# Performance work log

Hardware: AMD Instinct MI355X
Metric: run time of the kernel (lower is better)

Reference implementation:

```python
import jax, jax.numpy as jnp
import numpy as np
import math

EMBED_DIM = 1024
NHEAD = 16
HD = EMBED_DIM // NHEAD      # 64
HHD = HD // 2                # 32
LAMBDA_INIT = 0.8
LN_EPS = 1e-5
B, T = 2, 2048


def setup_inputs() -> dict:
    key = jax.random.key(0)
    ks = jax.random.split(key, 12)
    d = EMBED_DIM
    inp = {
        "x": jax.random.normal(ks[0], (B, T, d), dtype=jnp.float32),
        "key_padding_mask": jnp.zeros((B, T), dtype=bool),
        "Wq": jax.random.normal(ks[1], (d, d), dtype=jnp.float32) / math.sqrt(d),
        "Wk": jax.random.normal(ks[2], (d, d), dtype=jnp.float32) / math.sqrt(d),
        "Wv": jax.random.normal(ks[3], (d, d), dtype=jnp.float32) / math.sqrt(d),
        "Wo": jax.random.normal(ks[4], (d, d), dtype=jnp.float32) / math.sqrt(d),
        "gamma": jnp.ones((d,), dtype=jnp.float32),
        "beta": jnp.zeros((d,), dtype=jnp.float32),
        "lq1": jax.random.normal(ks[5], (NHEAD, HHD), dtype=jnp.float32) * 0.1,
        "lk1": jax.random.normal(ks[6], (NHEAD, HHD), dtype=jnp.float32) * 0.1,
        "lq2": jax.random.normal(ks[7], (NHEAD, HHD), dtype=jnp.float32) * 0.1,
        "lk2": jax.random.normal(ks[8], (NHEAD, HHD), dtype=jnp.float32) * 0.1,
    }
    return inp


def _diff_attn(x, key_padding_mask, Wq, Wk, Wv, Wo, gamma, beta, lq1, lk1, lq2, lk2):
    b, t, d = x.shape
    scale = math.sqrt(HHD)

    def split(w):  # [B,T,D] -> [B,H,T,hd]
        return w.reshape(b, t, NHEAD, HD).transpose(0, 2, 1, 3)

    Q = split(x @ Wq.T)
    K = split(x @ Wk.T)
    V = split(x @ Wv.T)
    Q1, Q2 = Q[..., :HHD], Q[..., HHD:]
    K1, K2 = K[..., :HHD], K[..., HHD:]

    def attn(q, k):  # [B,H,T,hhd] x [B,H,T,hhd] -> softmax scores [B,H,T,T]
        scores = jnp.einsum('bhqe,bhke->bhqk', q, k) / scale
        scores = jnp.where(key_padding_mask[:, None, None, :], -jnp.inf, scores)
        return jax.nn.softmax(scores, axis=-1)

    lam = (jnp.exp(jnp.sum(lq1 * lk1, axis=-1))
           - jnp.exp(jnp.sum(lq2 * lk2, axis=-1))
           + LAMBDA_INIT)  # [H]
    A = attn(Q1, K1) - lam[None, :, None, None] * attn(Q2, K2)
    out = jnp.einsum('bhqk,bhkd->bhqd', A, V).transpose(0, 2, 1, 3).reshape(b, t, d)
    y = out @ Wo.T + x
    mu = jnp.mean(y, axis=-1, keepdims=True)
    var = jnp.mean((y - mu) ** 2, axis=-1, keepdims=True)
    return (y - mu) / jnp.sqrt(var + LN_EPS) * gamma + beta


def reference(x, key_padding_mask, Wq, Wk, Wv, Wo, gamma, beta, lq1, lk1, lq2, lk2):
    return _diff_attn(x, key_padding_mask, Wq, Wk, Wv, Wo, gamma, beta, lq1, lk1, lq2, lk2)
```

## Files before the change

### kernel.cpp

```cpp
#include <hip/hip_runtime.h>
#include <stdint.h>

#define DEVI __device__ __forceinline__

typedef __bf16 bf16x8 __attribute__((ext_vector_type(8)));
typedef float f32x4 __attribute__((ext_vector_type(4)));
typedef unsigned short u16x8 __attribute__((ext_vector_type(8)));
typedef unsigned u32x2 __attribute__((ext_vector_type(2)));
typedef unsigned u32x4 __attribute__((ext_vector_type(4)));

#define MFMA16(a, b, c) __builtin_amdgcn_mfma_f32_16x16x32_bf16((a), (b), (c), 0, 0, 0)

constexpr int EMBED = 1024;
constexpr int NHEADC = 16;
constexpr int BB = 2;
constexpr int TT = 2048;
constexpr int MROWS = BB * TT;
constexpr int QKSTR = 2048;
constexpr float QSCALE = 0.17677669529663687f * 1.4426950408889634f;

DEVI unsigned short f2bf(float f) {
  unsigned u = __float_as_uint(f);
  u += 0x7fffu + ((u >> 16) & 1u);
  return (unsigned short)(u >> 16);
}
DEVI unsigned cvtpk(float lo, float hi) {
  unsigned pk;
  asm("v_cvt_pk_bf16_f32 %0, %1, %2" : "=v"(pk) : "v"(lo), "v"(hi));
  return pk;
}

DEVI void gl2lds16(const void* g, void* l) {
  __builtin_amdgcn_global_load_lds(
      (const __attribute__((address_space(1))) void*)(uintptr_t)g,
      (__attribute__((address_space(3))) void*)(unsigned)(uintptr_t)l,
      16, 0, 0);
}

DEVI void split_body(const float* in, unsigned short* hi, int n4, int start, int stride) {
  for (int i = start; i < n4; i += stride) {
    float4 v = reinterpret_cast<const float4*>(in)[i];
    ushort4 h;
    h.x = f2bf(v.x); h.y = f2bf(v.y); h.z = f2bf(v.z); h.w = f2bf(v.w);
    reinterpret_cast<ushort4*>(hi)[i] = h;
  }
}

__global__ __launch_bounds__(256) void k_split(const float* __restrict__ in,
                                               unsigned short* __restrict__ hi, int n4) {
  split_body(in, hi, n4, blockIdx.x * blockDim.x + threadIdx.x, gridDim.x * blockDim.x);
}

__global__ __launch_bounds__(256) void k_splitw(
    const float* __restrict__ Wq, const float* __restrict__ Wk,
    const float* __restrict__ Wv, const float* __restrict__ Wo,
    unsigned short* __restrict__ wqkv, unsigned short* __restrict__ woh) {
  const int y = blockIdx.y;
  const int n4 = EMBED * EMBED / 4;
  const float* in = (y == 0) ? Wq : (y == 1) ? Wk : (y == 2) ? Wv : Wo;
  unsigned short* hi =
      (y == 3) ? woh : wqkv + (size_t)y * EMBED * EMBED;
  split_body(in, hi, n4, blockIdx.x * blockDim.x + threadIdx.x, gridDim.x * blockDim.x);
}

template <int EPI>
__global__ __launch_bounds__(256) void k_gemm(
    const unsigned short* __restrict__ Ahi, const unsigned short* __restrict__ Bhi,
    unsigned short* __restrict__ O1, unsigned short* __restrict__ O2,
    float* __restrict__ Of32, const float* __restrict__ resid,
    int M, int N, int K, int ldo, float oscale) {
  __shared__ __align__(16) unsigned short sAh[128 * 64];
  __shared__ __align__(16) unsigned short sBh[128 * 64];

  const int tid = threadIdx.x;
  const int lane = tid & 63;
  const int w = tid >> 6;
  const int arow = lane & 15;
  const int g = lane >> 4;
  const int bm = blockIdx.y * 128;
  const int bn = blockIdx.x * 128;
  const int wr = (w >> 1) * 64;
  const int wc = (w & 1) * 64;

  const f32x4 z4 = {0.f, 0.f, 0.f, 0.f};
  f32x4 acc[4][4];
#pragma unroll
  for (int i = 0; i < 4; ++i)
#pragma unroll
    for (int j = 0; j < 4; ++j) acc[i][j] = z4;

  for (int k0 = 0; k0 < K; k0 += 64) {
    __syncthreads();
#pragma unroll
    for (int i = 0; i < 4; ++i) {
      const int cid = (i * 4 + w) * 64 + lane;
      const int r = cid >> 3;
      const int c = cid & 7;
      const int sc = (c ^ (r & 7)) * 8;
      const int ldso = (i * 4 + w) * 512;
      gl2lds16(Ahi + (size_t)(bm + r) * K + k0 + sc, &sAh[ldso]);
      gl2lds16(Bhi + (size_t)(bn + r) * K + k0 + sc, &sBh[ldso]);
    }
    __syncthreads();
#pragma unroll
    for (int kk = 0; kk < 2; ++kk) {
      bf16x8 ah[4], bh[4];
#pragma unroll
      for (int mi = 0; mi < 4; ++mi) {
        const int row = wr + mi * 16 + arow;
        const int ch = ((kk * 4 + g) ^ (row & 7)) * 8;
        ah[mi] = *reinterpret_cast<const bf16x8*>(&sAh[row * 64 + ch]);
      }
#pragma unroll
      for (int ni = 0; ni < 4; ++ni) {
        const int row = wc + ni * 16 + arow;
        const int ch = ((kk * 4 + g) ^ (row & 7)) * 8;
        bh[ni] = *reinterpret_cast<const bf16x8*>(&sBh[row * 64 + ch]);
      }
#pragma unroll
      for (int mi = 0; mi < 4; ++mi)
#pragma unroll
        for (int ni = 0; ni < 4; ++ni)
          acc[mi][ni] = MFMA16(ah[mi], bh[ni], acc[mi][ni]);
    }
  }

#pragma unroll
  for (int mi = 0; mi < 4; ++mi)
#pragma unroll
    for (int ni = 0; ni < 4; ++ni)
#pragma unroll
      for (int r = 0; r < 4; ++r) {
        const int row = bm + wr + mi * 16 + g * 4 + r;
        const int col = bn + wc + ni * 16 + arow;
        float f = acc[mi][ni][r];
        if constexpr (EPI == 2) {
          const size_t idx = (size_t)row * ldo + col;
          Of32[idx] = f + resid[idx];
        } else {
          if (col < 2048) {
            O1[(size_t)row * 2048 + col] = f2bf(col < 1024 ? f * oscale : f);
          } else {
            O2[(size_t)row * 1024 + (col - 2048)] = f2bf(f);
          }
        }
      }
}

__global__ __launch_bounds__(256, 4) void k_attn(
    const unsigned short* __restrict__ QKhi, const unsigned short* __restrict__ Vb,
    unsigned short* __restrict__ Out,
    const float* __restrict__ lq1, const float* __restrict__ lk1,
    const float* __restrict__ lq2, const float* __restrict__ lk2) {
  __shared__ __align__(16) unsigned short sK[2][64 * 64];
  __shared__ __align__(16) unsigned short sVt[64 * 64];

  const int tid = threadIdx.x;
  const int lane = tid & 63;
  const int w = tid >> 6;
  const int ten = w >> 1;
  const int qc = w & 1;
  const int arow = lane & 15;
  const int g = lane >> 4;
  const int a3 = arow >> 3;

  const int lin = blockIdx.x;
  const int m_ = lin >> 3;
  const int bh = ((m_ >> 6) << 3) | (lin & 7);
  const int qx = m_ & 63;
  const int q0 = qx * 32;
  const int b = bh >> 4;
  const int h = bh & 15;

  const int r0 = tid >> 3;
  const int c0 = tid & 7;
  const unsigned short* kg =
      QKhi + (size_t)(b * TT + r0) * QKSTR + 1024 + h * 64 + ((c0 ^ (r0 & 7)) * 8);
  const size_t kgj = (size_t)32 * QKSTR;
  unsigned short* const kda = &sK[0][w * 512];
  unsigned short* const kdb = &sK[0][2048 + w * 512];

  const int tp = tid >> 3;
  const int vc = tid & 7;
  const unsigned short* vg = Vb + (size_t)(b * TT + 2 * tp) * EMBED + h * 64 + vc * 8;
  unsigned vwoff[8];
#pragma unroll
  for (int i = 0; i < 8; ++i)
    vwoff[i] = (vc * 8 + i) * 128 + ((tp ^ (((i ^ (vc & 3)) & 7) << 2)) << 2);

  const char* const kfb = reinterpret_cast<const char*>(&sK[0][0]) + arow * 128 +
                          (((g + 4 * ten) ^ (arow & 7)) * 16);
  const char* const svt = reinterpret_cast<const char*>(sVt);
  const int s0 = (arow & 7) ^ (a3 & 3);
  const int s1 = (arow & 7) ^ ((2 + a3) & 3);
  const char* const vf00 = svt + arow * 128 + ((g ^ s0) * 16);
  const char* const vf01 = svt + arow * 128 + (((4 + g) ^ s0) * 16);
  const char* const vf10 = svt + (16 + arow) * 128 + ((g ^ s1) * 16);
  const char* const vf11 = svt + (16 + arow) * 128 + (((4 + g) ^ s1) * 16);

  u16x8 va0, va1, na0, na1;
  gl2lds16(kg, kda);
  gl2lds16(kg + kgj, kdb);
  va0 = *reinterpret_cast<const u16x8*>(vg);
  va1 = *reinterpret_cast<const u16x8*>(vg + EMBED);
  kg += (size_t)64 * QKSTR;
  vg += (size_t)64 * EMBED;

  const int qrow = q0 + qc * 16 + arow;
  const bf16x8 qh = *reinterpret_cast<const bf16x8*>(
      &QKhi[(size_t)(b * TT + qrow) * QKSTR + h * 64 + ten * 32 + g * 8]);

  float d1 = 0.f, d2 = 0.f;
#pragma unroll
  for (int i = 0; i < 32; ++i) {
    d1 += lq1[h * 32 + i] * lk1[h * 32 + i];
    d2 += lq2[h * 32 + i] * lk2[h * 32 + i];
  }
  const float lam = __expf(d1) - __expf(d2) + 0.8f;

  const f32x4 z4 = {0.f, 0.f, 0.f, 0.f};
  f32x4 o[4];
  float ls0 = 0.f, ls1 = 0.f;
#pragma unroll
  for (int n = 0; n < 4; ++n) o[n] = z4;

#define ATTN_TILE(T, KOFF, KDa, KDb)                                                 \
  do {                                                                               \
    __syncthreads();                  \
    if ((T) + 1 < TT / 64) {                                                         \
      gl2lds16(kg, (KDa));                                                           \
      gl2lds16(kg + kgj, (KDb));                                                     \
      na0 = *reinterpret_cast<const u16x8*>(vg);                                     \
      na1 = *reinterpret_cast<const u16x8*>(vg + EMBED);                             \
      kg += (size_t)64 * QKSTR;                                                      \
      vg += (size_t)64 * EMBED;                                                      \
      asm volatile("s_waitcnt vmcnt(4)" ::: "memory");                               \
    } else {                                                                         \
      asm volatile("s_waitcnt vmcnt(0)" ::: "memory");                               \
    }                                                                                \
    {                   \
      char* vb8 = reinterpret_cast<char*>(sVt);                                      \
      const u32x4 pd0 = __builtin_bit_cast(u32x4, va0);                              \
      const u32x4 pd1 = __builtin_bit_cast(u32x4, va1);                              \
      _Pragma("unroll") for (int dw = 0; dw < 4; ++dw) {                             \
        const unsigned pe = __builtin_amdgcn_perm(pd1[dw], pd0[dw], 0x05040100);     \
        const unsigned po = __builtin_amdgcn_perm(pd1[dw], pd0[dw], 0x07060302);     \
        *reinterpret_cast<unsigned*>(vb8 + vwoff[2 * dw]) = pe;                      \
        *reinterpret_cast<unsigned*>(vb8 + vwoff[2 * dw + 1]) = po;                  \
      }                                                                              \
    }                                                                                \
    __syncthreads();                                                \
    f32x4 s[4];                                                                      \
    __builtin_amdgcn_s_setprio(1);                                                   \
    _Pragma("unroll") for (int n = 0; n < 4; ++n) {                                  \
      const bf16x8 kh =                                                              \
          *reinterpret_cast<const bf16x8*>(kfb + (KOFF) + n * 2048);                 \
      s[n] = MFMA16(kh, qh, z4);                                                     \
    }                                                                                \
    __builtin_amdgcn_s_setprio(0);                                                   \
    unsigned pk[4][2];                                                               \
    _Pragma("unroll") for (int n = 0; n < 4; ++n) {                                  \
      const float p0 = __builtin_amdgcn_exp2f(s[n][0]);                              \
      const float p1 = __builtin_amdgcn_exp2f(s[n][1]);                              \
      const float p2 = __builtin_amdgcn_exp2f(s[n][2]);                              \
      const float p3 = __builtin_amdgcn_exp2f(s[n][3]);                              \
      ls0 += p0 + p1;                                                                \
      ls1 += p2 + p3;                                                                \
      pk[n][0] = cvtpk(p0, p1);                                                      \
      pk[n][1] = cvtpk(p2, p3);                                                      \
    }                                                                                \
    bf16x8 pf[2];                                                                    \
    _Pragma("unroll") for (int kk = 0; kk < 2; ++kk) {                               \
      unsigned u0 = pk[2 * kk][0], w0 = pk[2 * kk + 1][0];                           \
      asm("v_permlane32_swap_b32 %0, %1" : "+v"(u0), "+v"(w0));                      \
      asm("v_permlane16_swap_b32 %0, %1" : "+v"(u0), "+v"(w0));                      \
      unsigned u1 = pk[2 * kk][1], w1 = pk[2 * kk + 1][1];                           \
      asm("v_permlane32_swap_b32 %0, %1" : "+v"(u1), "+v"(w1));                      \
      asm("v_permlane16_swap_b32 %0, %1" : "+v"(u1), "+v"(w1));                      \
      const u32x4 q4 = {u0, u1, w0, w1};                                             \
      pf[kk] = __builtin_bit_cast(bf16x8, q4);                                       \
    }                                                                                \
    __builtin_amdgcn_s_setprio(1);                                                   \
    _Pragma("unroll") for (int n = 0; n < 4; ++n) {                                  \
      const int half = (n >> 1) * 4096;                                              \
      const bf16x8 vfa = *reinterpret_cast<const bf16x8*>(                           \
          ((n & 1) ? vf10 : vf00) + half);                                           \
      o[n] = MFMA16(vfa, pf[0], o[n]);                                               \
      const bf16x8 vfb2 = *reinterpret_cast<const bf16x8*>(                          \
          ((n & 1) ? vf11 : vf01) + half);                                           \
      o[n] = MFMA16(vfb2, pf[1], o[n]);                                              \
    }                                                                                \
    __builtin_amdgcn_s_setprio(0);                                                   \
    va0 = na0;                                                                       \
    va1 = na1;                                                                       \
  } while (0)

  for (int tt = 0; tt < TT / 128; ++tt) {
    ATTN_TILE(2 * tt, 0, kda + 4096, kdb + 4096);
    ATTN_TILE(2 * tt + 1, 8192, kda, kdb);
  }
#undef ATTN_TILE

  float lsum = ls0 + ls1;
  lsum += __shfl_xor(lsum, 16, 64);
  lsum += __shfl_xor(lsum, 32, 64);

  float* sComb = reinterpret_cast<float*>(&sK[0][0]);
  __syncthreads();
  if (ten == 1) {
    const float rl2 = lam / lsum;
#pragma unroll
    for (int n = 0; n < 4; ++n)
#pragma unroll
      for (int r = 0; r < 4; ++r)
        sComb[(qc * 16 + arow) * 72 + n * 16 + g * 4 + r] = o[n][r] * rl2;
  }
  __syncthreads();
  if (ten == 0) {
    const float rl1 = 1.f / lsum;
    const size_t orow = (size_t)(b * TT + q0 + qc * 16 + arow) * EMBED + h * 64;
    const float* cb = &sComb[(qc * 16 + arow) * 72];
#pragma unroll
    for (int n = 0; n < 4; ++n) {
      const float v0 = o[n][0] * rl1 - cb[n * 16 + g * 4 + 0];
      const float v1 = o[n][1] * rl1 - cb[n * 16 + g * 4 + 1];
      const float v2 = o[n][2] * rl1 - cb[n * 16 + g * 4 + 2];
      const float v3 = o[n][3] * rl1 - cb[n * 16 + g * 4 + 3];
      u32x2 pk2;
      pk2[0] = cvtpk(v0, v1);
      pk2[1] = cvtpk(v2, v3);
      *reinterpret_cast<u32x2*>(&Out[orow + n * 16 + g * 4]) = pk2;
    }
  }
}

__global__ __launch_bounds__(256) void k_ln(const float* __restrict__ y,
                                            const float* __restrict__ gamma,
                                            const float* __restrict__ beta,
                                            float* __restrict__ out) {
  __shared__ float red[2][4];
  const int row = blockIdx.x;
  const int tid = threadIdx.x;
  const int lane = tid & 63;
  const int w = tid >> 6;
  float4 v = reinterpret_cast<const float4*>(y + (size_t)row * 1024)[tid];
  float s = v.x + v.y + v.z + v.w;
  float q = v.x * v.x + v.y * v.y + v.z * v.z + v.w * v.w;
#pragma unroll
  for (int mask = 32; mask >= 1; mask >>= 1) {
    s += __shfl_xor(s, mask, 64);
    q += __shfl_xor(q, mask, 64);
  }
  if (lane == 0) { red[0][w] = s; red[1][w] = q; }
  __syncthreads();
  s = red[0][0] + red[0][1] + red[0][2] + red[0][3];
  q = red[1][0] + red[1][1] + red[1][2] + red[1][3];
  const float mu = s * (1.f / 1024.f);
  const float var = q * (1.f / 1024.f) - mu * mu;
  const float rstd = rsqrtf(var + 1e-5f);
  const float4 gm = reinterpret_cast<const float4*>(gamma)[tid];
  const float4 bt = reinterpret_cast<const float4*>(beta)[tid];
  float4 o;
  o.x = (v.x - mu) * rstd * gm.x + bt.x;
  o.y = (v.y - mu) * rstd * gm.y + bt.y;
  o.z = (v.z - mu) * rstd * gm.z + bt.z;
  o.w = (v.w - mu) * rstd * gm.w + bt.w;
  reinterpret_cast<float4*>(out + (size_t)row * 1024)[tid] = o;
}

extern "C" void kernel_launch(void* const* d_in, const int* in_sizes, int n_in,
                              void* d_out, int out_size, void* d_ws, size_t ws_size,
                              hipStream_t stream) {
  const float* x = (const float*)d_in[0];
  const float* Wq = (const float*)d_in[2];
  const float* Wk = (const float*)d_in[3];
  const float* Wv = (const float*)d_in[4];
  const float* Wo = (const float*)d_in[5];
  const float* gamma = (const float*)d_in[6];
  const float* beta = (const float*)d_in[7];
  const float* lq1 = (const float*)d_in[8];
  const float* lk1 = (const float*)d_in[9];
  const float* lq2 = (const float*)d_in[10];
  const float* lk2 = (const float*)d_in[11];

  size_t off = 0;
  auto wsalloc = [&](size_t bytes) -> void* {
    void* p = (char*)d_ws + off;
    off += (bytes + 255) & ~(size_t)255;
    return p;
  };
  const size_t actb = (size_t)MROWS * EMBED * 2;
  const size_t wtb = (size_t)EMBED * EMBED * 2;
  const size_t qkb = (size_t)MROWS * QKSTR * 2;
  unsigned short* xhi = (unsigned short*)wsalloc(actb);
  unsigned short* wqkv = (unsigned short*)wsalloc(3 * wtb);
  unsigned short* woh = (unsigned short*)wsalloc(wtb);
  unsigned short* qkh = (unsigned short*)wsalloc(qkb);
  unsigned short* vb = (unsigned short*)wsalloc(actb);
  unsigned short* ao = (unsigned short*)wsalloc(actb);
  float* yf = (float*)wsalloc((size_t)MROWS * EMBED * 4);

  k_split<<<1024, 256, 0, stream>>>(x, xhi, MROWS * EMBED / 4);
  k_splitw<<<dim3(128, 4), 256, 0, stream>>>(Wq, Wk, Wv, Wo, wqkv, woh);

  k_gemm<4><<<dim3(24, 32), 256, 0, stream>>>(
      xhi, wqkv, qkh, vb, nullptr, nullptr, MROWS, 3072, EMBED, 0, QSCALE);

  k_attn<<<2048, 256, 0, stream>>>(qkh, vb, ao, lq1, lk1, lq2, lk2);

  k_gemm<2><<<dim3(8, 32), 256, 0, stream>>>(
      ao, woh, nullptr, nullptr, yf, x, MROWS, 1024, EMBED, 1024, 1.f);

  k_ln<<<MROWS, 256, 0, stream>>>(yf, gamma, beta, (float*)d_out);
}
```

Before: 168.2 us.

## Process 64 query rows per attention block to reuse K/V tiles

Each attention workgroup now covers 64 query rows instead of 32, with each wave holding two Q fragments and two sets of output accumulators. Every K and V tile staged into LDS therefore feeds twice as many queries, and the grid is halved to 1024 blocks. This cuts global K/V reads and LDS staging work per query. In exchange it raises register pressure per wave, enlarges shared memory, and halves the number of blocks, which may reduce occupancy and latency hiding.

```diff
diff --git a/kernel.cpp b/kernel.cpp
--- a/kernel.cpp
+++ b/kernel.cpp
@@ -152,8 +152,7 @@
     unsigned short* __restrict__ Out,
     const float* __restrict__ lq1, const float* __restrict__ lk1,
     const float* __restrict__ lq2, const float* __restrict__ lk2) {
-  __shared__ __align__(16) unsigned short sK[2][64 * 64];
-  __shared__ __align__(16) unsigned short sVt[64 * 64];
+  __shared__ __align__(16) char sPool[36864];
 
   const int tid = threadIdx.x;
   const int lane = tid & 63;
@@ -166,9 +165,9 @@
 
   const int lin = blockIdx.x;
   const int m_ = lin >> 3;
-  const int bh = ((m_ >> 6) << 3) | (lin & 7);
-  const int qx = m_ & 63;
-  const int q0 = qx * 32;
+  const int bh = ((m_ >> 5) << 3) | (lin & 7);
+  const int qx = m_ & 31;
+  const int q0 = qx * 64;
   const int b = bh >> 4;
   const int h = bh & 15;
 
@@ -177,8 +176,8 @@
   const unsigned short* kg =
       QKhi + (size_t)(b * TT + r0) * QKSTR + 1024 + h * 64 + ((c0 ^ (r0 & 7)) * 8);
   const size_t kgj = (size_t)32 * QKSTR;
-  unsigned short* const kda = &sK[0][w * 512];
-  unsigned short* const kdb = &sK[0][2048 + w * 512];
+  unsigned short* const kda = reinterpret_cast<unsigned short*>(sPool + w * 1024);
+  unsigned short* const kdb = reinterpret_cast<unsigned short*>(sPool + 4096 + w * 1024);
 
   const int tp = tid >> 3;
   const int vc = tid & 7;
@@ -186,11 +185,11 @@
   unsigned vwoff[8];
 #pragma unroll
   for (int i = 0; i < 8; ++i)
-    vwoff[i] = (vc * 8 + i) * 128 + ((tp ^ (((i ^ (vc & 3)) & 7) << 2)) << 2);
-
-  const char* const kfb = reinterpret_cast<const char*>(&sK[0][0]) + arow * 128 +
-                          (((g + 4 * ten) ^ (arow & 7)) * 16);
-  const char* const svt = reinterpret_cast<const char*>(sVt);
+    vwoff[i] = 16384 + (vc * 8 + i) * 128 + ((tp ^ (((i ^ (vc & 3)) & 7) << 2)) << 2);
+
+  const char* const kfb =
+      sPool + arow * 128 + (((g + 4 * ten) ^ (arow & 7)) * 16);
+  const char* const svt = sPool + 16384;
   const int s0 = (arow & 7) ^ (a3 & 3);
   const int s1 = (arow & 7) ^ ((2 + a3) & 3);
   const char* const vf00 = svt + arow * 128 + ((g ^ s0) * 16);
@@ -206,9 +205,10 @@
   kg += (size_t)64 * QKSTR;
   vg += (size_t)64 * EMBED;
 
-  const int qrow = q0 + qc * 16 + arow;
-  const bf16x8 qh = *reinterpret_cast<const bf16x8*>(
-      &QKhi[(size_t)(b * TT + qrow) * QKSTR + h * 64 + ten * 32 + g * 8]);
+  const size_t qrb =
+      (size_t)(b * TT + q0 + qc * 32 + arow) * QKSTR + h * 64 + ten * 32 + g * 8;
+  const bf16x8 qh0 = *reinterpret_cast<const bf16x8*>(&QKhi[qrb]);
+  const bf16x8 qh1 = *reinterpret_cast<const bf16x8*>(&QKhi[qrb + 16 * QKSTR]);
 
   float d1 = 0.f, d2 = 0.f;
 #pragma unroll
@@ -219,10 +219,10 @@
   const float lam = __expf(d1) - __expf(d2) + 0.8f;
 
   const f32x4 z4 = {0.f, 0.f, 0.f, 0.f};
-  f32x4 o[4];
+  f32x4 o0[4], o1[4];
   float ls0 = 0.f, ls1 = 0.f;
 #pragma unroll
-  for (int n = 0; n < 4; ++n) o[n] = z4;
+  for (int n = 0; n < 4; ++n) { o0[n] = z4; o1[n] = z4; }
 
 #define ATTN_TILE(T, KOFF, KDa, KDb)                                                 \
   do {                                                                               \
@@ -239,56 +239,58 @@
       asm volatile("s_waitcnt vmcnt(0)" ::: "memory");                               \
     }                                                                                \
     {                   \
-      char* vb8 = reinterpret_cast<char*>(sVt);                                      \
       const u32x4 pd0 = __builtin_bit_cast(u32x4, va0);                              \
       const u32x4 pd1 = __builtin_bit_cast(u32x4, va1);                              \
       _Pragma("unroll") for (int dw = 0; dw < 4; ++dw) {                             \
         const unsigned pe = __builtin_amdgcn_perm(pd1[dw], pd0[dw], 0x05040100);     \
         const unsigned po = __builtin_amdgcn_perm(pd1[dw], pd0[dw], 0x07060302);     \
-        *reinterpret_cast<unsigned*>(vb8 + vwoff[2 * dw]) = pe;                      \
-        *reinterpret_cast<unsigned*>(vb8 + vwoff[2 * dw + 1]) = po;                  \
+        *reinterpret_cast<unsigned*>(sPool + vwoff[2 * dw]) = pe;                    \
+        *reinterpret_cast<unsigned*>(sPool + vwoff[2 * dw + 1]) = po;                \
       }                                                                              \
     }                                                                                \
     __syncthreads();                                                \
-    f32x4 s[4];                                                                      \
-    __builtin_amdgcn_s_setprio(1);                                                   \
-    _Pragma("unroll") for (int n = 0; n < 4; ++n) {                                  \
-      const bf16x8 kh =                                                              \
-          *reinterpret_cast<const bf16x8*>(kfb + (KOFF) + n * 2048);                 \
-      s[n] = MFMA16(kh, qh, z4);                                                     \
-    }                                                                                \
-    __builtin_amdgcn_s_setprio(0);                                                   \
-    unsigned pk[4][2];                                                               \
-    _Pragma("unroll") for (int n = 0; n < 4; ++n) {                                  \
-      const float p0 = __builtin_amdgcn_exp2f(s[n][0]);                              \
-      const float p1 = __builtin_amdgcn_exp2f(s[n][1]);                              \
-      const float p2 = __builtin_amdgcn_exp2f(s[n][2]);                              \
-      const float p3 = __builtin_amdgcn_exp2f(s[n][3]);                              \
-      ls0 += p0 + p1;                                                                \
-      ls1 += p2 + p3;                                                                \
-      pk[n][0] = cvtpk(p0, p1);                                                      \
-      pk[n][1] = cvtpk(p2, p3);                                                      \
-    }                                                                                \
-    bf16x8 pf[2];                                                                    \
-    _Pragma("unroll") for (int kk = 0; kk < 2; ++kk) {                               \
-      unsigned u0 = pk[2 * kk][0], w0 = pk[2 * kk + 1][0];                           \
-      asm("v_permlane32_swap_b32 %0, %1" : "+v"(u0), "+v"(w0));                      \
-      asm("v_permlane16_swap_b32 %0, %1" : "+v"(u0), "+v"(w0));                      \
-      unsigned u1 = pk[2 * kk][1], w1 = pk[2 * kk + 1][1];                           \
-      asm("v_permlane32_swap_b32 %0, %1" : "+v"(u1), "+v"(w1));                      \
-      asm("v_permlane16_swap_b32 %0, %1" : "+v"(u1), "+v"(w1));                      \
-      const u32x4 q4 = {u0, u1, w0, w1};                                             \
-      pf[kk] = __builtin_bit_cast(bf16x8, q4);                                       \
+    bf16x8 khv[4];                                                                   \
+    _Pragma("unroll") for (int n = 0; n < 4; ++n)                                    \
+        khv[n] = *reinterpret_cast<const bf16x8*>(kfb + (KOFF) + n * 2048);          \
+    bf16x8 pf[2][2];                                                                 \
+    _Pragma("unroll") for (int qg = 0; qg < 2; ++qg) {                               \
+      f32x4 s_[4];                                                                   \
+      __builtin_amdgcn_s_setprio(1);                                                 \
+      _Pragma("unroll") for (int n = 0; n < 4; ++n)                                  \
+          s_[n] = MFMA16(khv[n], (qg == 0) ? qh0 : qh1, z4);                         \
+      __builtin_amdgcn_s_setprio(0);                                                 \
+      unsigned pk_[4][2];                                                            \
+      _Pragma("unroll") for (int n = 0; n < 4; ++n) {                                \
+        const float p0 = __builtin_amdgcn_exp2f(s_[n][0]);                           \
+        const float p1 = __builtin_amdgcn_exp2f(s_[n][1]);                           \
+        const float p2 = __builtin_amdgcn_exp2f(s_[n][2]);                           \
+        const float p3 = __builtin_amdgcn_exp2f(s_[n][3]);                           \
+        ((qg == 0) ? ls0 : ls1) += (p0 + p1) + (p2 + p3);                            \
+        pk_[n][0] = cvtpk(p0, p1);                                                   \
+        pk_[n][1] = cvtpk(p2, p3);                                                   \
+      }                                                                              \
+      _Pragma("unroll") for (int kk = 0; kk < 2; ++kk) {                             \
+        unsigned u0 = pk_[2 * kk][0], w0 = pk_[2 * kk + 1][0];                       \
+        asm("v_permlane32_swap_b32 %0, %1" : "+v"(u0), "+v"(w0));                    \
+        asm("v_permlane16_swap_b32 %0, %1" : "+v"(u0), "+v"(w0));                    \
+        unsigned u1 = pk_[2 * kk][1], w1 = pk_[2 * kk + 1][1];                       \
+        asm("v_permlane32_swap_b32 %0, %1" : "+v"(u1), "+v"(w1));                    \
+        asm("v_permlane16_swap_b32 %0, %1" : "+v"(u1), "+v"(w1));                    \
+        const u32x4 q4 = {u0, u1, w0, w1};                                           \
+        pf[qg][kk] = __builtin_bit_cast(bf16x8, q4);                                 \
+      }                                                                              \
     }                                                                                \
     __builtin_amdgcn_s_setprio(1);                                                   \
     _Pragma("unroll") for (int n = 0; n < 4; ++n) {                                  \
       const int half = (n >> 1) * 4096;                                              \
       const bf16x8 vfa = *reinterpret_cast<const bf16x8*>(                           \
           ((n & 1) ? vf10 : vf00) + half);                                           \
-      o[n] = MFMA16(vfa, pf[0], o[n]);                                               \
+      o0[n] = MFMA16(vfa, pf[0][0], o0[n]);                                          \
+      o1[n] = MFMA16(vfa, pf[1][0], o1[n]);                                          \
       const bf16x8 vfb2 = *reinterpret_cast<const bf16x8*>(                          \
           ((n & 1) ? vf11 : vf01) + half);                                           \
-      o[n] = MFMA16(vfb2, pf[1], o[n]);                                              \
+      o0[n] = MFMA16(vfb2, pf[0][1], o0[n]);                                         \
+      o1[n] = MFMA16(vfb2, pf[1][1], o1[n]);                                         \
     }                                                                                \
     __builtin_amdgcn_s_setprio(0);                                                   \
     va0 = na0;                                                                       \
@@ -301,25 +303,24 @@
   }
 #undef ATTN_TILE
 
-  float lsum = ls0 + ls1;
-  lsum += __shfl_xor(lsum, 16, 64);
-  lsum += __shfl_xor(lsum, 32, 64);
-
-  float* sComb = reinterpret_cast<float*>(&sK[0][0]);
-  __syncthreads();
-  if (ten == 1) {
-    const float rl2 = lam / lsum;
+  ls0 += __shfl_xor(ls0, 16, 64);
+  ls0 += __shfl_xor(ls0, 32, 64);
+  ls1 += __shfl_xor(ls1, 16, 64);
+  ls1 += __shfl_xor(ls1, 32, 64);
+
+  float* sComb = reinterpret_cast<float*>(sPool);
+  auto deposit = [&](const f32x4 (&o)[4], float l, int row) {
+    const float rl2 = lam / l;
 #pragma unroll
     for (int n = 0; n < 4; ++n)
 #pragma unroll
       for (int r = 0; r < 4; ++r)
-        sComb[(qc * 16 + arow) * 72 + n * 16 + g * 4 + r] = o[n][r] * rl2;
-  }
-  __syncthreads();
-  if (ten == 0) {
-    const float rl1 = 1.f / lsum;
-    const size_t orow = (size_t)(b * TT + q0 + qc * 16 + arow) * EMBED + h * 64;
-    const float* cb = &sComb[(qc * 16 + arow) * 72];
+        sComb[row * 72 + n * 16 + g * 4 + r] = o[n][r] * rl2;
+  };
+  auto emit = [&](const f32x4 (&o)[4], float l, int row) {
+    const float rl1 = 1.f / l;
+    const float* cb = &sComb[row * 72];
+    const size_t orow = (size_t)(b * TT + q0 + row) * EMBED + h * 64;
 #pragma unroll
     for (int n = 0; n < 4; ++n) {
       const float v0 = o[n][0] * rl1 - cb[n * 16 + g * 4 + 0];
@@ -331,6 +332,16 @@
       pk2[1] = cvtpk(v2, v3);
       *reinterpret_cast<u32x2*>(&Out[orow + n * 16 + g * 4]) = pk2;
     }
+  };
+  __syncthreads();
+  if (ten == 1) {
+    deposit(o0, ls0, qc * 32 + arow);
+    deposit(o1, ls1, qc * 32 + 16 + arow);
+  }
+  __syncthreads();
+  if (ten == 0) {
+    emit(o0, ls0, qc * 32 + arow);
+    emit(o1, ls1, qc * 32 + 16 + arow);
   }
 }
 
@@ -406,7 +417,7 @@
   k_gemm<4><<<dim3(24, 32), 256, 0, stream>>>(
       xhi, wqkv, qkh, vb, nullptr, nullptr, MROWS, 3072, EMBED, 0, QSCALE);
 
-  k_attn<<<2048, 256, 0, stream>>>(qkh, vb, ao, lq1, lk1, lq2, lk2);
+  k_attn<<<1024, 256, 0, stream>>>(qkh, vb, ao, lq1, lk1, lq2, lk2);
 
   k_gemm<2><<<dim3(8, 32), 256, 0, stream>>>(
       ao, woh, nullptr, nullptr, yf, x, MROWS, 1024, EMBED, 1024, 1.f);
```

Result: slower. 335.0 us (+99.2%).
